# Optimization experiments

Hardware: AMD Instinct MI355X
Metric: run time of the kernel (lower is better)

The kernel has to match this reference:

```python
import jax, jax.numpy as jnp
import numpy as np

B, N, D = 4, 2048, 1024
DF = 4 * D
EPS = 1e-5


def _layernorm(x, w, b):
    mu = jnp.mean(x, axis=-1, keepdims=True)
    var = jnp.mean(jnp.square(x - mu), axis=-1, keepdims=True)
    return (x - mu) * jax.lax.rsqrt(var + EPS) * w + b


def setup_inputs() -> dict:
    key = jax.random.key(0)
    ks = jax.random.split(key, 8)
    x = jax.random.normal(ks[0], (B, N, D), dtype=jnp.float32)
    # conv filter param (torch init is zeros; use small randn for numeric coverage)
    weights = jax.random.normal(ks[1], (1, 1, N), dtype=jnp.float32) * 0.02
    # registered buffer: sqrt(1/(i+1)) per token, shape (1, N, 1)
    scale = jnp.sqrt(1.0 / (jnp.arange(N, dtype=jnp.float32) + 1.0))[None, :, None]
    ln1_w = jnp.ones((D,), jnp.float32)
    ln1_b = jnp.zeros((D,), jnp.float32)
    W1 = jax.random.normal(ks[2], (DF, D), dtype=jnp.float32) * 0.02
    b1 = jnp.zeros((DF,), jnp.float32)
    W2 = jax.random.normal(ks[3], (D, DF), dtype=jnp.float32) * 0.02
    b2 = jnp.zeros((D,), jnp.float32)
    scalar = jax.random.normal(ks[4], (1,), dtype=jnp.float32) * 0.1
    ln2_w = jnp.ones((D,), jnp.float32)
    ln2_b = jnp.zeros((D,), jnp.float32)
    return dict(x=x, weights=weights, scale=scale, ln1_w=ln1_w, ln1_b=ln1_b,
                W1=W1, b1=b1, W2=W2, b2=b2, scalar=scalar, ln2_w=ln2_w, ln2_b=ln2_b)


def reference(x, weights, scale, ln1_w, ln1_b, W1, b1, W2, b2, scalar, ln2_w, ln2_b):
    n = weights.shape[-1]
    # FFT token-mixing conv: operate over token axis. x: (B,N,D) -> (B,D,N)
    xt = jnp.swapaxes(x, -2, -1)
    # real inputs -> rfft/irfft equals real(ifft(fft*fft)) from the torch code
    prod = jnp.fft.rfft(xt, n=2 * n) * jnp.fft.rfft(weights, n=2 * n)
    conv = jnp.fft.irfft(prod, n=2 * n)[..., :n]  # (B,D,N)
    x1 = jnp.swapaxes(conv, -2, -1)               # (B,N,D)
    x1 = _layernorm(x + x1 * scale, ln1_w, ln1_b)
    # GELU MLP (torch F.gelu default = exact erf gelu)
    h = jax.nn.gelu(jnp.einsum('bnd,fd->bnf', x1, W1) + b1, approximate=False)
    mlp = jnp.einsum('bnf,df->bnd', h, W2) + b2
    x2 = _layernorm(x1 + scalar * mlp, ln2_w, ln2_b)
    return x2
```

## Files before the change

kernel.cpp:

```cpp
#include <hip/hip_runtime.h>
#include <cstdint>

typedef float floatx4 __attribute__((ext_vector_type(4)));
typedef int intx8 __attribute__((ext_vector_type(8)));

__device__ __forceinline__ unsigned short f2b(float f) {
  union { float f; unsigned u; } v; v.f = f;
  return (unsigned short)((v.u + 0x7FFFu + ((v.u >> 16) & 1u)) >> 16);
}
__device__ __forceinline__ float b2f(unsigned short h) {
  union { unsigned u; float f; } v; v.u = ((unsigned)h) << 16;
  return v.f;
}

__device__ __forceinline__ void gload_lds16(const void* g, void* l) {
  __builtin_amdgcn_global_load_lds(
      (const __attribute__((address_space(1))) void*)g,
      (__attribute__((address_space(3))) void*)l, 16, 0, 0);
}


__global__ void cast_f8x64_kernel(const float* __restrict__ in,
                                  int* __restrict__ out) {
  long i = (long)blockIdx.x * 256 + threadIdx.x;
  float4 v = ((const float4*)in)[i];
  int pk = __builtin_amdgcn_cvt_pk_fp8_f32(v.x * 64.0f, v.y * 64.0f, 0, false);
  pk = __builtin_amdgcn_cvt_pk_fp8_f32(v.z * 64.0f, v.w * 64.0f, pk, true);
  out[i] = pk;
}

__global__ void build_T8_kernel(const float* __restrict__ w,
                                int* __restrict__ T8) {
  long i = (long)blockIdx.x * 256 + threadIdx.x;
  int n = (int)(i >> 9);
  int m0 = (int)(i & 511) * 4;
  float v[4];
#pragma unroll
  for (int r = 0; r < 4; ++r) {
    int m = m0 + r;
    v[r] = (m <= n) ? w[n - m] * 64.0f : 0.0f;
  }
  int pk = __builtin_amdgcn_cvt_pk_fp8_f32(v[0], v[1], 0, false);
  pk = __builtin_amdgcn_cvt_pk_fp8_f32(v[2], v[3], pk, true);
  T8[i] = pk;
}

__global__ void transpose_cast_f8_kernel(const float* __restrict__ x,
                                         unsigned char* __restrict__ xT) {
  __shared__ float tile[32][33];
  int b = blockIdx.z;
  int n0 = blockIdx.y * 32;
  int d0 = blockIdx.x * 32;
  int tx = threadIdx.x;
  int ty = threadIdx.y;
  for (int i = ty; i < 32; i += 8)
    tile[i][tx] = x[((long)b * 2048 + n0 + i) * 1024 + d0 + tx];
  __syncthreads();
  float a = tile[ty * 4 + 0][tx];
  float c = tile[ty * 4 + 1][tx];
  float e = tile[ty * 4 + 2][tx];
  float f = tile[ty * 4 + 3][tx];
  int pk = __builtin_amdgcn_cvt_pk_fp8_f32(a, c, 0, false);
  pk = __builtin_amdgcn_cvt_pk_fp8_f32(e, f, pk, true);
  *(int*)(xT + ((long)b * 1024 + d0 + tx) * 2048 + n0 + ty * 4) = pk;
}

template <int EPI, int NT, bool TRI>
__global__ __launch_bounds__(256, 4) void gemm_f8(
    const unsigned char* __restrict__ A, const unsigned char* __restrict__ B,
    int Kstride, int Kloop, long zsA, long zsB, long zsC,
    int rx, int ryb, int gxn, unsigned sclA, unsigned sclB,
    const float* __restrict__ resid, const float* __restrict__ scale,
    const float* __restrict__ bias,
    float* __restrict__ Cf, unsigned short* __restrict__ Cb,
    unsigned char* __restrict__ C8) {
  __shared__ __align__(16) unsigned char As[16 * 1040];
  __shared__ __align__(16) unsigned char Bs[16 * 1040];
  const int tid = threadIdx.x;
  const int wid = tid >> 6;
  const int lane = tid & 63;
  const int quad = lane >> 4;
  const int l16 = lane & 15;
  const int wm = (wid >> 1) * 64;
  const int wn = (wid & 1) * 64;

  const int bid = blockIdx.x;
  const int xcd = bid & 7;
  const int ib = bid >> 3;
  const int ci = ib % rx;
  const int ri = ib / rx;
  long bm, bn;
  if (TRI) {
    bm = (long)(ri == 0 ? xcd : 15 - xcd) * 128;
    bn = (long)ci * 128;
  } else {
    const int gx = xcd % gxn;
    const int gy = xcd / gxn;
    bm = (long)(gy * ryb + ri) * 128;
    bn = (long)(gx * rx + ci) * 128;
  }
  const int bz = blockIdx.z;
  const unsigned char* Ab = A + zsA * bz;
  const unsigned char* Bb = B + zsB * bz;

  floatx4 acc[4][4];
#pragma unroll
  for (int i = 0; i < 4; ++i)
#pragma unroll
    for (int j = 0; j < 4; ++j)
      acc[i][j] = floatx4{0.0f, 0.0f, 0.0f, 0.0f};

  const int srow = tid >> 3;
  const int scol = (tid & 7) * 16;
  const unsigned char* gA[4];
  const unsigned char* gB[4];
  unsigned char* lA[4];
  unsigned char* lB[4];
#pragma unroll
  for (int p = 0; p < 4; ++p) {
    gA[p] = Ab + (bm + p * 32 + srow) * (long)Kstride + scol;
    gB[p] = Bb + (bn + p * 32 + srow) * (long)Kstride + scol;
    lA[p] = As + (p * 4 + wid) * 1040;
    lB[p] = Bs + (p * 4 + wid) * 1040;
  }

  const int kend = TRI ? min(Kloop, (int)bm + 128) : Kloop;
  for (int kk = 0; kk < kend; kk += 128) {
    __syncthreads();
#pragma unroll
    for (int p = 0; p < 4; ++p) {
      gload_lds16(gA[p] + kk, lA[p]);
      gload_lds16(gB[p] + kk, lB[p]);
    }
    __syncthreads();
    intx8 af[4], bfr[4];
#pragma unroll
    for (int i = 0; i < 4; ++i) {
      const int ra = wm + i * 16 + l16;
      const int off = (ra >> 3) * 1040 + (ra & 7) * 128 + quad * 32;
      union { intx8 v; int4 q[2]; } u;
      u.q[0] = *(const int4*)(As + off);
      u.q[1] = *(const int4*)(As + off + 16);
      af[i] = u.v;
    }
#pragma unroll
    for (int j = 0; j < 4; ++j) {
      const int rb = wn + j * 16 + l16;
      const int off = (rb >> 3) * 1040 + (rb & 7) * 128 + quad * 32;
      union { intx8 v; int4 q[2]; } u;
      u.q[0] = *(const int4*)(Bs + off);
      u.q[1] = *(const int4*)(Bs + off + 16);
      bfr[j] = u.v;
    }
#pragma unroll
    for (int i = 0; i < 4; ++i)
#pragma unroll
      for (int j = 0; j < 4; ++j)
        acc[i][j] = __builtin_amdgcn_mfma_scale_f32_16x16x128_f8f6f4(
            af[i], bfr[j], acc[i][j], 0 , 0 ,
            0, sclA, 0, sclB);
  }

#pragma unroll
  for (int i = 0; i < 4; ++i)
#pragma unroll
    for (int j = 0; j < 4; ++j)
#pragma unroll
      for (int r = 0; r < 4; ++r) {
        long row = bm + wm + i * 16 + quad * 4 + r;
        long col = bn + wn + j * 16 + l16;
        long idx = (long)bz * zsC + row * (long)NT + col;
        float v = acc[i][j][r];
        if (EPI == 0) {
          Cb[idx] = f2b(v);
        } else if (EPI == 1) {
          Cf[idx] = resid[idx] + scale[row] * v;
        } else {
          v += bias[col];
          float u = v * (0.7978845608f + 0.0356774081f * v * v);
          float u2 = u * u;
          float t = __fdividef(u * (15.0f + u2), 15.0f + 6.0f * u2);
          t = fminf(fmaxf(t, -1.0f), 1.0f);
          float g = 0.5f * v * (1.0f + t);
          int pk = __builtin_amdgcn_cvt_pk_fp8_f32(g, 0.0f, 0, false);
          C8[idx] = (unsigned char)(pk & 0xFF);
        }
      }
}

__global__ __launch_bounds__(256) void ln_kernel(
    const float* __restrict__ in, const float* __restrict__ w,
    const float* __restrict__ b, unsigned short* __restrict__ outb,
    int* __restrict__ outf8) {
  const long row = blockIdx.x;
  const int tid = threadIdx.x;
  float4 v = ((const float4*)in)[row * 256 + tid];
  float s = v.x + v.y + v.z + v.w;
  float ss = v.x * v.x + v.y * v.y + v.z * v.z + v.w * v.w;
#pragma unroll
  for (int off = 32; off > 0; off >>= 1) {
    s += __shfl_down(s, off);
    ss += __shfl_down(ss, off);
  }
  __shared__ float red[8];
  const int wid = tid >> 6, lane = tid & 63;
  if (lane == 0) { red[wid] = s; red[4 + wid] = ss; }
  __syncthreads();
  s = red[0] + red[1] + red[2] + red[3];
  ss = red[4] + red[5] + red[6] + red[7];
  const float mu = s * (1.0f / 1024.0f);
  const float var = ss * (1.0f / 1024.0f) - mu * mu;
  const float rs = rsqrtf(var + 1e-5f);
  float4 wv = ((const float4*)w)[tid];
  float4 bv = ((const float4*)b)[tid];
  float o0 = (v.x - mu) * rs * wv.x + bv.x;
  float o1 = (v.y - mu) * rs * wv.y + bv.y;
  float o2 = (v.z - mu) * rs * wv.z + bv.z;
  float o3 = (v.w - mu) * rs * wv.w + bv.w;
  ushort4 u{f2b(o0), f2b(o1), f2b(o2), f2b(o3)};
  ((ushort4*)outb)[row * 256 + tid] = u;
  int pk = __builtin_amdgcn_cvt_pk_fp8_f32(o0, o1, 0, false);
  pk = __builtin_amdgcn_cvt_pk_fp8_f32(o2, o3, pk, true);
  outf8[row * 256 + tid] = pk;
}

__global__ __launch_bounds__(256) void ln2_fused_kernel(
    const unsigned short* __restrict__ y0, const unsigned short* __restrict__ y1,
    const unsigned short* __restrict__ x1b, const float* __restrict__ b2,
    const float* __restrict__ scalar_p, const float* __restrict__ w,
    const float* __restrict__ b, float* __restrict__ out) {
  const long row = blockIdx.x;
  const int tid = threadIdx.x;
  ushort4 a4 = ((const ushort4*)y0)[row * 256 + tid];
  ushort4 c4 = ((const ushort4*)y1)[row * 256 + tid];
  ushort4 xr = ((const ushort4*)x1b)[row * 256 + tid];
  float4 bias = ((const float4*)b2)[tid];
  const float scl = scalar_p[0];
  float4 v;
  v.x = b2f(xr.x) + scl * (b2f(a4.x) + b2f(c4.x) + bias.x);
  v.y = b2f(xr.y) + scl * (b2f(a4.y) + b2f(c4.y) + bias.y);
  v.z = b2f(xr.z) + scl * (b2f(a4.z) + b2f(c4.z) + bias.z);
  v.w = b2f(xr.w) + scl * (b2f(a4.w) + b2f(c4.w) + bias.w);
  float s = v.x + v.y + v.z + v.w;
  float ss = v.x * v.x + v.y * v.y + v.z * v.z + v.w * v.w;
#pragma unroll
  for (int off = 32; off > 0; off >>= 1) {
    s += __shfl_down(s, off);
    ss += __shfl_down(ss, off);
  }
  __shared__ float red[8];
  const int wid = tid >> 6, lane = tid & 63;
  if (lane == 0) { red[wid] = s; red[4 + wid] = ss; }
  __syncthreads();
  s = red[0] + red[1] + red[2] + red[3];
  ss = red[4] + red[5] + red[6] + red[7];
  const float mu = s * (1.0f / 1024.0f);
  const float var = ss * (1.0f / 1024.0f) - mu * mu;
  const float rs = rsqrtf(var + 1e-5f);
  float4 wv = ((const float4*)w)[tid];
  float4 bv = ((const float4*)b)[tid];
  float4 o;
  o.x = (v.x - mu) * rs * wv.x + bv.x;
  o.y = (v.y - mu) * rs * wv.y + bv.y;
  o.z = (v.z - mu) * rs * wv.z + bv.z;
  o.w = (v.w - mu) * rs * wv.w + bv.w;
  ((float4*)out)[row * 256 + tid] = o;
}

extern "C" void kernel_launch(void* const* d_in, const int* in_sizes, int n_in,
                              void* d_out, int out_size, void* d_ws, size_t ws_size,
                              hipStream_t stream) {
  const float* x      = (const float*)d_in[0];
  const float* wconv  = (const float*)d_in[1];
  const float* scale  = (const float*)d_in[2];
  const float* ln1w   = (const float*)d_in[3];
  const float* ln1b   = (const float*)d_in[4];
  const float* W1     = (const float*)d_in[5];
  const float* b1     = (const float*)d_in[6];
  const float* W2     = (const float*)d_in[7];
  const float* b2     = (const float*)d_in[8];
  const float* scalar = (const float*)d_in[9];
  const float* ln2w   = (const float*)d_in[10];
  const float* ln2b   = (const float*)d_in[11];
  float* out = (float*)d_out;

  const unsigned SCL_1  = 0x7F7F7F7Fu;
  const unsigned SCL_64 = 0x79797979u;

  char* ws = (char*)d_ws;
  unsigned char* xT8   = (unsigned char*)ws;  ws += (size_t)4 * 1024 * 2048;
  unsigned char* T8    = (unsigned char*)ws;  ws += (size_t)2048 * 2048;
  unsigned char* W1f8  = (unsigned char*)ws;  ws += (size_t)4096 * 1024;
  unsigned char* W2f8  = (unsigned char*)ws;  ws += (size_t)4096 * 1024;
  float* y             = (float*)ws;          ws += (size_t)8192 * 1024 * 4;
  unsigned short* yb   = (unsigned short*)ws; ws += (size_t)2 * 8192 * 1024 * 2;
  unsigned short* x1b  = (unsigned short*)ws; ws += (size_t)8192 * 1024 * 2;
  unsigned char* x1f8  = (unsigned char*)ws;  ws += (size_t)8192 * 1024;
  unsigned char* h8    = (unsigned char*)ws;  ws += (size_t)8192 * 4096;

  cast_f8x64_kernel<<<4096, 256, 0, stream>>>(W1, (int*)W1f8);
  cast_f8x64_kernel<<<4096, 256, 0, stream>>>(W2, (int*)W2f8);
  build_T8_kernel<<<4096, 256, 0, stream>>>(wconv, (int*)T8);
  transpose_cast_f8_kernel<<<dim3(32, 64, 4), dim3(32, 8), 0, stream>>>(x, xT8);

  gemm_f8<1, 1024, true><<<dim3(128, 1, 4), 256, 0, stream>>>(
      T8, xT8, 2048, 2048, 0L, (long)1024 * 2048, (long)2048 * 1024,
      8, 0, 0, SCL_64, SCL_1, x, scale, nullptr, y, nullptr, nullptr);
  ln_kernel<<<8192, 256, 0, stream>>>(y, ln1w, ln1b, x1b, (int*)x1f8);
  gemm_f8<2, 4096, false><<<dim3(2048, 1, 1), 256, 0, stream>>>(
      x1f8, W1f8, 1024, 1024, 0L, 0L, 0L,
      16, 16, 2, SCL_1, SCL_64, nullptr, nullptr, b1, nullptr, nullptr, h8);
  gemm_f8<0, 1024, false><<<dim3(512, 1, 2), 256, 0, stream>>>(
      h8, W2f8, 4096, 2048, 2048L, 2048L, (long)8192 * 1024,
      8, 8, 1, SCL_1, SCL_64, nullptr, nullptr, nullptr, nullptr, yb, nullptr);
  ln2_fused_kernel<<<8192, 256, 0, stream>>>(
      yb, yb + (size_t)8192 * 1024, x1b, b2, scalar, ln2w, ln2b, out);
}
```

Before: 293.3 us.

## Double-buffer LDS tiles in FP8 GEMM to overlap global loads with MFMA

The FP8 GEMM main loop now keeps two LDS buffers. It issues the direct-to-LDS global loads for the next K tile before computing on the current one, and uses vmcnt waits plus raw barriers in place of the two __syncthreads. LDS offsets are precomputed, and the MFMA block is wrapped in s_setprio to favour matrix issue. Doubling LDS to about 66KB lowers the occupancy hint from 4 to 2 blocks per CU, so latency hiding now comes from the software pipeline instead of extra resident waves.

```diff
diff --git a/kernel.cpp b/kernel.cpp
--- a/kernel.cpp
+++ b/kernel.cpp
@@ -66,7 +66,7 @@
 }
 
 template <int EPI, int NT, bool TRI>
-__global__ __launch_bounds__(256, 4) void gemm_f8(
+__global__ __launch_bounds__(256, 2) void gemm_f8(
     const unsigned char* __restrict__ A, const unsigned char* __restrict__ B,
     int Kstride, int Kloop, long zsA, long zsB, long zsC,
     int rx, int ryb, int gxn, unsigned sclA, unsigned sclB,
@@ -74,8 +74,8 @@
     const float* __restrict__ bias,
     float* __restrict__ Cf, unsigned short* __restrict__ Cb,
     unsigned char* __restrict__ C8) {
-  __shared__ __align__(16) unsigned char As[16 * 1040];
-  __shared__ __align__(16) unsigned char Bs[16 * 1040];
+  __shared__ __align__(16) unsigned char As[2 * 16 * 1040];
+  __shared__ __align__(16) unsigned char Bs[2 * 16 * 1040];
   const int tid = threadIdx.x;
   const int wid = tid >> 6;
   const int lane = tid & 63;
@@ -124,34 +124,55 @@
     lB[p] = Bs + (p * 4 + wid) * 1040;
   }
 
+  int offA[4], offB[4];
+#pragma unroll
+  for (int i = 0; i < 4; ++i) {
+    const int ra = wm + i * 16 + l16;
+    offA[i] = (ra >> 3) * 1040 + (ra & 7) * 128 + quad * 32;
+    const int rb = wn + i * 16 + l16;
+    offB[i] = (rb >> 3) * 1040 + (rb & 7) * 128 + quad * 32;
+  }
+
   const int kend = TRI ? min(Kloop, (int)bm + 128) : Kloop;
+
+#pragma unroll
+  for (int p = 0; p < 4; ++p) {
+    gload_lds16(gA[p], lA[p]);
+    gload_lds16(gB[p], lB[p]);
+  }
+
+  int so = 0;
   for (int kk = 0; kk < kend; kk += 128) {
-    __syncthreads();
-#pragma unroll
-    for (int p = 0; p < 4; ++p) {
-      gload_lds16(gA[p] + kk, lA[p]);
-      gload_lds16(gB[p] + kk, lB[p]);
+    const int kn = kk + 128;
+    if (kn < kend) {
+      const int po = so ^ 16640;
+#pragma unroll
+      for (int p = 0; p < 4; ++p) {
+        gload_lds16(gA[p] + kn, lA[p] + po);
+        gload_lds16(gB[p] + kn, lB[p] + po);
+      }
+      asm volatile("s_waitcnt vmcnt(8)" ::: "memory");
+    } else {
+      asm volatile("s_waitcnt vmcnt(0)" ::: "memory");
     }
-    __syncthreads();
+    __builtin_amdgcn_s_barrier();
+
     intx8 af[4], bfr[4];
 #pragma unroll
     for (int i = 0; i < 4; ++i) {
-      const int ra = wm + i * 16 + l16;
-      const int off = (ra >> 3) * 1040 + (ra & 7) * 128 + quad * 32;
       union { intx8 v; int4 q[2]; } u;
-      u.q[0] = *(const int4*)(As + off);
-      u.q[1] = *(const int4*)(As + off + 16);
+      u.q[0] = *(const int4*)(As + so + offA[i]);
+      u.q[1] = *(const int4*)(As + so + offA[i] + 16);
       af[i] = u.v;
     }
 #pragma unroll
     for (int j = 0; j < 4; ++j) {
-      const int rb = wn + j * 16 + l16;
-      const int off = (rb >> 3) * 1040 + (rb & 7) * 128 + quad * 32;
       union { intx8 v; int4 q[2]; } u;
-      u.q[0] = *(const int4*)(Bs + off);
-      u.q[1] = *(const int4*)(Bs + off + 16);
+      u.q[0] = *(const int4*)(Bs + so + offB[j]);
+      u.q[1] = *(const int4*)(Bs + so + offB[j] + 16);
       bfr[j] = u.v;
     }
+    __builtin_amdgcn_s_setprio(1);
 #pragma unroll
     for (int i = 0; i < 4; ++i)
 #pragma unroll
@@ -159,6 +180,9 @@
         acc[i][j] = __builtin_amdgcn_mfma_scale_f32_16x16x128_f8f6f4(
             af[i], bfr[j], acc[i][j], 0 , 0 ,
             0, sclA, 0, sclB);
+    __builtin_amdgcn_s_setprio(0);
+    __builtin_amdgcn_s_barrier();
+    so ^= 16640;
   }
 
 #pragma unroll
```

Result: no change. 297.9 us (+1.6%).

## Switch FP8 GEMM to 32x32x64 scaled MFMA with XOR-swizzled LDS layout

Applied to the files above, without the earlier changes.

Replaces the 16x16x128 scaled FP8 MFMA tiles with 32x32x64 MFMAs, so each wave computes a 2x2 grid of 32x32 accumulators instead of 4x4 grid of 16x16. The global-to-LDS column placement and LDS read offsets are XOR-swizzled to avoid bank conflicts for the new access pattern. Fewer LDS fragment reads per MFMA and larger MFMA instructions aim to raise matrix-core utilization; the swizzle and epilogue row mapping must match the 32x32 output layout exactly or results will be wrong.

```diff
diff --git a/kernel.cpp b/kernel.cpp
--- a/kernel.cpp
+++ b/kernel.cpp
@@ -2,6 +2,7 @@
 #include <cstdint>
 
 typedef float floatx4 __attribute__((ext_vector_type(4)));
+typedef float floatx16 __attribute__((ext_vector_type(16)));
 typedef int intx8 __attribute__((ext_vector_type(8)));
 
 __device__ __forceinline__ unsigned short f2b(float f) {
@@ -17,6 +18,20 @@
   __builtin_amdgcn_global_load_lds(
       (const __attribute__((address_space(1))) void*)g,
       (__attribute__((address_space(3))) void*)l, 16, 0, 0);
+}
+
+__device__ __forceinline__ intx8 lds_read32(const unsigned char* p) {
+  union { intx8 v; int4 q[2]; } u;
+  u.q[0] = *(const int4*)p;
+  u.q[1] = *(const int4*)(p + 16);
+  return u.v;
+}
+
+__device__ __forceinline__ int swz_scol(int lane) {
+  const int q = (lane >> 1) & 3;
+  const int r3 = (lane >> 3) & 3;
+  const int sbit = lane & 1;
+  return ((((q ^ r3) << 1) | sbit) << 4);
 }
 
 
@@ -79,8 +94,8 @@
   const int tid = threadIdx.x;
   const int wid = tid >> 6;
   const int lane = tid & 63;
-  const int quad = lane >> 4;
-  const int l16 = lane & 15;
+  const int l32 = lane & 31;
+  const int half = lane >> 5;
   const int wm = (wid >> 1) * 64;
   const int wn = (wid & 1) * 64;
 
@@ -103,15 +118,16 @@
   const unsigned char* Ab = A + zsA * bz;
   const unsigned char* Bb = B + zsB * bz;
 
-  floatx4 acc[4][4];
-#pragma unroll
-  for (int i = 0; i < 4; ++i)
-#pragma unroll
-    for (int j = 0; j < 4; ++j)
-      acc[i][j] = floatx4{0.0f, 0.0f, 0.0f, 0.0f};
+  floatx16 acc[2][2];
+#pragma unroll
+  for (int i = 0; i < 2; ++i)
+#pragma unroll
+    for (int j = 0; j < 2; ++j)
+#pragma unroll
+      for (int e = 0; e < 16; ++e) acc[i][j][e] = 0.0f;
 
   const int srow = tid >> 3;
-  const int scol = (tid & 7) * 16;
+  const int scol = swz_scol(lane);
   const unsigned char* gA[4];
   const unsigned char* gB[4];
   unsigned char* lA[4];
@@ -124,6 +140,19 @@
     lB[p] = Bs + (p * 4 + wid) * 1040;
   }
 
+  int offA[2][2], offB[2][2];
+#pragma unroll
+  for (int i = 0; i < 2; ++i)
+#pragma unroll
+    for (int s = 0; s < 2; ++s) {
+      const int ra = wm + i * 32 + l32;
+      const int ca = (s * 2 + half) ^ (ra & 3);
+      offA[i][s] = (ra >> 3) * 1040 + (ra & 7) * 128 + (ca << 5);
+      const int rb = wn + i * 32 + l32;
+      const int cb = (s * 2 + half) ^ (rb & 3);
+      offB[i][s] = (rb >> 3) * 1040 + (rb & 7) * 128 + (cb << 5);
+    }
+
   const int kend = TRI ? min(Kloop, (int)bm + 128) : Kloop;
   for (int kk = 0; kk < kend; kk += 128) {
     __syncthreads();
@@ -133,42 +162,31 @@
       gload_lds16(gB[p] + kk, lB[p]);
     }
     __syncthreads();
-    intx8 af[4], bfr[4];
-#pragma unroll
-    for (int i = 0; i < 4; ++i) {
-      const int ra = wm + i * 16 + l16;
-      const int off = (ra >> 3) * 1040 + (ra & 7) * 128 + quad * 32;
-      union { intx8 v; int4 q[2]; } u;
-      u.q[0] = *(const int4*)(As + off);
-      u.q[1] = *(const int4*)(As + off + 16);
-      af[i] = u.v;
+#pragma unroll
+    for (int s = 0; s < 2; ++s) {
+      intx8 b0 = lds_read32(Bs + offB[0][s]);
+      intx8 b1 = lds_read32(Bs + offB[1][s]);
+      intx8 a0 = lds_read32(As + offA[0][s]);
+      intx8 a1 = lds_read32(As + offA[1][s]);
+      acc[0][0] = __builtin_amdgcn_mfma_scale_f32_32x32x64_f8f6f4(
+          a0, b0, acc[0][0], 0, 0, 0, sclA, 0, sclB);
+      acc[0][1] = __builtin_amdgcn_mfma_scale_f32_32x32x64_f8f6f4(
+          a0, b1, acc[0][1], 0, 0, 0, sclA, 0, sclB);
+      acc[1][0] = __builtin_amdgcn_mfma_scale_f32_32x32x64_f8f6f4(
+          a1, b0, acc[1][0], 0, 0, 0, sclA, 0, sclB);
+      acc[1][1] = __builtin_amdgcn_mfma_scale_f32_32x32x64_f8f6f4(
+          a1, b1, acc[1][1], 0, 0, 0, sclA, 0, sclB);
     }
-#pragma unroll
-    for (int j = 0; j < 4; ++j) {
-      const int rb = wn + j * 16 + l16;
-      const int off = (rb >> 3) * 1040 + (rb & 7) * 128 + quad * 32;
-      union { intx8 v; int4 q[2]; } u;
-      u.q[0] = *(const int4*)(Bs + off);
-      u.q[1] = *(const int4*)(Bs + off + 16);
-      bfr[j] = u.v;
-    }
-#pragma unroll
-    for (int i = 0; i < 4; ++i)
-#pragma unroll
-      for (int j = 0; j < 4; ++j)
-        acc[i][j] = __builtin_amdgcn_mfma_scale_f32_16x16x128_f8f6f4(
-            af[i], bfr[j], acc[i][j], 0 , 0 ,
-            0, sclA, 0, sclB);
-  }
-
-#pragma unroll
-  for (int i = 0; i < 4; ++i)
-#pragma unroll
-    for (int j = 0; j < 4; ++j)
-#pragma unroll
-      for (int r = 0; r < 4; ++r) {
-        long row = bm + wm + i * 16 + quad * 4 + r;
-        long col = bn + wn + j * 16 + l16;
+  }
+
+#pragma unroll
+  for (int i = 0; i < 2; ++i)
+#pragma unroll
+    for (int j = 0; j < 2; ++j)
+#pragma unroll
+      for (int r = 0; r < 16; ++r) {
+        long row = bm + wm + i * 32 + (r & 3) + 8 * (r >> 2) + 4 * half;
+        long col = bn + wn + j * 32 + l32;
         long idx = (long)bz * zsC + row * (long)NT + col;
         float v = acc[i][j][r];
         if (EPI == 0) {
```

Result: no change. 298.8 us (+1.9%).
